# Performance work log

Measured on AMD Instinct MI355X. Metric: run time of the kernel, lower is better.

Reference implementation:

```python
import jax, jax.numpy as jnp
import numpy as np

L = 2000          # number of residues (sequence length)
FEATURES_L = 2048 # config.features_L pad target
W = 7             # config.window_size
D = 54            # per-residue feature dim after bert_lin
H = 3             # attention heads
HD = D // H       # head dim = 18
CH = 32           # conv hidden channels
KS = (3, 5, 7)    # config.kernels


def setup_inputs() -> dict:
    key = jax.random.key(0)
    ks = jax.random.split(key, 20)
    n = lambda k, s, sc=0.02: jax.random.normal(k, s, jnp.float32) * sc
    return {
        'beft_f': jax.random.normal(ks[0], (L, 1024), jnp.float32),
        'pssm_f': jax.random.normal(ks[1], (L, 20), jnp.float32),
        'hmm_f': jax.random.normal(ks[2], (L, 30), jnp.float32),
        'dssp_f': jax.random.normal(ks[3], (L, 14), jnp.float32),
        'W_bert': n(ks[4], (1024, D)), 'b_bert': jnp.zeros((D,), jnp.float32),
        'ln_g1': jnp.ones((D,), jnp.float32), 'ln_b1': jnp.zeros((D,), jnp.float32),
        'ln_g2': jnp.ones((D,), jnp.float32), 'ln_b2': jnp.zeros((D,), jnp.float32),
        'conv1_w': n(ks[5], (CH, 1, 3, 1), 0.1), 'conv1_b': n(ks[6], (CH,), 0.1),
        'prelu_a': jnp.array(0.25, jnp.float32),
        'conv2_w': n(ks[7], (CH, 1, 5, 1), 0.1), 'conv2_b': n(ks[8], (CH,), 0.1),
        'conv3_w': n(ks[9], (CH, 1, 7, 1), 0.1), 'conv3_b': n(ks[10], (CH,), 0.1),
        'W1': n(ks[11], (972, 256)), 'b1': jnp.zeros((256,), jnp.float32),
        'W2': n(ks[12], (CH * 256, 256)), 'b2': jnp.zeros((256,), jnp.float32),
    }


def _ln(x, g, b, eps=1e-5):
    m = x.mean(-1, keepdims=True)
    v = ((x - m) ** 2).mean(-1, keepdims=True)
    return (x - m) * jax.lax.rsqrt(v + eps) * g + b


def _attn(x, g, b):
    # x: (L, W, D); no qkv projections, no 1/sqrt(d) scaling (as in source)
    qh = x.reshape(x.shape[0], W, H, HD)
    s = jnp.einsum('bqhd,bkhd->bhqk', qh, qh)
    p = jax.nn.softmax(s, axis=-1)
    o = jnp.einsum('bhqk,bkhd->bqhd', p, qh).reshape(x.shape[0], W, D)
    return _ln(o, g, b)


def _conv_branch(x, w, bias, k, act):
    pad = (k - 1) // 2
    c = jax.lax.conv_general_dilated(x, w, (1, 1), ((pad, pad), (0, 0)),
                                     dimension_numbers=('NCHW', 'OIHW', 'NCHW'))
    c = act(c + bias[None, :, None, None])
    c = jax.lax.reduce_window(c, -jnp.inf, jax.lax.max,
                              (1, 1, k, 1), (1, 1, 1, 1), 'VALID')
    return c.reshape(c.shape[0], CH, -1)  # (FEATURES_L, 32, (W-k+1)*2D)


def _forward(beft_f, W_bert, b_bert, ln_g1, ln_b1, ln_g2, ln_b2,
             conv1_w, conv1_b, prelu_a, conv2_w, conv2_b, conv3_w, conv3_b,
             W1, b1, W2, b2):
    f = beft_f @ W_bert + b_bert  # (L, 54)
    # sliding-window gather replicating the source python loop exactly:
    # interior rows i in (W, L-W): window = f[i-4 : i+3]; boundary rows: [f[i], 0...0]
    i = jnp.arange(L)
    j = jnp.arange(W)
    gidx = jnp.clip(i[:, None] - (W // 2 + 1) + j[None, :], 0, L - 1)
    win_int = f[gidx]                                   # (L, 7, 54)
    win_bnd = jnp.zeros((L, W, D), f.dtype).at[:, 0].set(f)
    boundary = (i <= W) | (i + W >= L)
    new_f = jnp.where(boundary[:, None, None], win_bnd, win_int)
    sf = _attn(new_f, ln_g1, ln_b1)
    sf = _attn(sf, ln_g2, ln_b2)
    cat = jnp.concatenate([new_f, sf], axis=2)          # (L, 7, 108)
    x = jnp.pad(cat, ((0, FEATURES_L - L), (0, 0), (0, 0)))[:, None]  # (FL,1,7,108)
    prelu = lambda z: jnp.where(z >= 0, z, prelu_a * z)
    feats = jnp.concatenate([
        _conv_branch(x, conv1_w, conv1_b, KS[0], prelu),
        _conv_branch(x, conv2_w, conv2_b, KS[1], jax.nn.relu),
        _conv_branch(x, conv3_w, conv3_b, KS[2], jax.nn.relu)], axis=2)  # (FL,32,972)
    y = feats[:L] @ W1 + b1                             # (L, 32, 256)
    y = y.reshape(L, CH * 256) @ W2 + b2                # (L, 256)
    return jnp.where(y >= 0, y, 0.01 * y)               # leaky_relu


def reference(beft_f, pssm_f, hmm_f, dssp_f, W_bert, b_bert, ln_g1, ln_b1,
              ln_g2, ln_b2, conv1_w, conv1_b, prelu_a, conv2_w, conv2_b,
              conv3_w, conv3_b, W1, b1, W2, b2):
    # pssm_f / hmm_f / dssp_f are accepted but unused in the source forward
    return _forward(beft_f, W_bert, b_bert, ln_g1, ln_b1, ln_g2, ln_b2,
                    conv1_w, conv1_b, prelu_a, conv2_w, conv2_b,
                    conv3_w, conv3_b, W1, b1, W2, b2)
```

## Files before the change

### kernel.cpp

```cpp
#include <hip/hip_runtime.h>

#define L_RES 2000
#define DF 54
#define WIN 7

typedef short bf16x8 __attribute__((ext_vector_type(8)));
typedef float f32x4 __attribute__((ext_vector_type(4)));
typedef unsigned short ushort8v __attribute__((ext_vector_type(8)));

__device__ __forceinline__ unsigned short f2bf(float f) {
    unsigned int u = __float_as_uint(f);
    unsigned int r = (u + 0x7FFFu + ((u >> 16) & 1u)) >> 16;
    return (unsigned short)r;
}
__device__ __forceinline__ float bf2f(unsigned short h) {
    return __uint_as_float(((unsigned int)h) << 16);
}
__device__ __forceinline__ void gload16(const unsigned short* g, unsigned short* l) {
    __builtin_amdgcn_global_load_lds(
        (const __attribute__((address_space(1))) void*)g,
        (__attribute__((address_space(3))) void*)l, 16, 0, 0);
}

__global__ __launch_bounds__(256) void split_beft(const float* __restrict__ beft,
                                                  unsigned short* __restrict__ A2) {
    int l = blockIdx.x;
    int t = threadIdx.x;
    unsigned short* row = A2 + (size_t)l * 3072;
    for (int k = t; k < 1024; k += 256) {
        unsigned short hi = 0, lo = 0;
        if (l < L_RES) {
            float x = beft[(size_t)l * 1024 + k];
            hi = f2bf(x);
            lo = f2bf(x - bf2f(hi));
        }
        row[k] = hi;
        row[1024 + k] = lo;
        row[2048 + k] = hi;
    }
}

__global__ __launch_bounds__(256) void b2t_build(const float* __restrict__ Wb,
                                                 unsigned short* __restrict__ B2T) {
    int idx = blockIdx.x * 256 + threadIdx.x;
    int n = idx / 3072, col = idx % 3072;
    int seg = col >> 10, k = col & 1023;
    unsigned short r = 0;
    if (n < DF) {
        float v = Wb[(size_t)k * DF + n];
        unsigned short hi = f2bf(v);
        r = (seg < 2) ? hi : f2bf(v - bf2f(hi));
    }
    B2T[idx] = r;
}

__global__ __launch_bounds__(256) void bert_mfma(const unsigned short* __restrict__ A2,
                                                 const unsigned short* __restrict__ B2T,
                                                 float* __restrict__ bpart) {
    __shared__ unsigned short ldsA[128 * 64];
    __shared__ unsigned short ldsB[64 * 64];
    int t = threadIdx.x, w = t >> 6, lane = t & 63;
    int m0 = blockIdx.x * 128;
    int z = blockIdx.y;
    long koff = (long)z * 768;
    int wr = w >> 1, wc = w & 1;
    int arow = lane & 15, kgrp = lane >> 4;

    const unsigned short* aS[4]; const unsigned short* bS[2];
    int aD[4], bD[2];
    #pragma unroll
    for (int j = 0; j < 4; ++j) {
        int s = j * 256 + t, r = s >> 3, c = s & 7;
        aS[j] = A2 + koff + (size_t)(m0 + r) * 3072 + c * 8;
        aD[j] = r * 64 + ((c ^ (r & 7)) * 8);
    }
    #pragma unroll
    for (int j = 0; j < 2; ++j) {
        int s = j * 256 + t, r = s >> 3, c = s & 7;
        bS[j] = B2T + koff + (size_t)r * 3072 + c * 8;
        bD[j] = r * 64 + ((c ^ (r & 7)) * 8);
    }
    f32x4 acc[4][2];
    #pragma unroll
    for (int mi = 0; mi < 4; ++mi)
        #pragma unroll
        for (int ni = 0; ni < 2; ++ni) acc[mi][ni] = (f32x4)(0.f);

    ushort8v va[4], vb[2];
    #pragma unroll
    for (int j = 0; j < 4; ++j) va[j] = *(const ushort8v*)(aS[j]);
    #pragma unroll
    for (int j = 0; j < 2; ++j) vb[j] = *(const ushort8v*)(bS[j]);

    for (int ks = 0; ks < 12; ++ks) {
        __syncthreads();
        #pragma unroll
        for (int j = 0; j < 4; ++j) *(ushort8v*)&ldsA[aD[j]] = va[j];
        #pragma unroll
        for (int j = 0; j < 2; ++j) *(ushort8v*)&ldsB[bD[j]] = vb[j];
        __syncthreads();
        if (ks + 1 < 12) {
            #pragma unroll
            for (int j = 0; j < 4; ++j) va[j] = *(const ushort8v*)(aS[j] + (ks + 1) * 64);
            #pragma unroll
            for (int j = 0; j < 2; ++j) vb[j] = *(const ushort8v*)(bS[j] + (ks + 1) * 64);
        }
        #pragma unroll
        for (int kk = 0; kk < 2; ++kk) {
            int chunk = kk * 4 + kgrp;
            bf16x8 af[4], bfr[2];
            #pragma unroll
            for (int mi = 0; mi < 4; ++mi) {
                int rl = wr * 64 + mi * 16 + arow;
                af[mi] = *(const bf16x8*)&ldsA[rl * 64 + ((chunk ^ (rl & 7)) * 8)];
            }
            #pragma unroll
            for (int ni = 0; ni < 2; ++ni) {
                int rl = wc * 32 + ni * 16 + arow;
                bfr[ni] = *(const bf16x8*)&ldsB[rl * 64 + ((chunk ^ (rl & 7)) * 8)];
            }
            #pragma unroll
            for (int mi = 0; mi < 4; ++mi)
                #pragma unroll
                for (int ni = 0; ni < 2; ++ni)
                    acc[mi][ni] = __builtin_amdgcn_mfma_f32_16x16x32_bf16(af[mi], bfr[ni], acc[mi][ni], 0, 0, 0);
        }
    }
    #pragma unroll
    for (int ni = 0; ni < 2; ++ni) {
        int n = wc * 32 + ni * 16 + arow;
        #pragma unroll
        for (int mi = 0; mi < 4; ++mi)
            #pragma unroll
            for (int r = 0; r < 4; ++r) {
                int m = m0 + wr * 64 + mi * 16 + kgrp * 4 + r;
                bpart[((size_t)z * 2048 + m) * 64 + n] = acc[mi][ni][r];
            }
    }
}

__global__ __launch_bounds__(64) void bert_reduce(const float* __restrict__ bpart,
                                                  const float* __restrict__ bb,
                                                  float* __restrict__ f) {
    int l = blockIdx.x, n = threadIdx.x;
    if (n < DF) {
        float s = bb[n];
        #pragma unroll
        for (int z = 0; z < 4; ++z) s += bpart[((size_t)z * 2048 + l) * 64 + n];
        f[(size_t)l * DF + n] = s;
    }
}

__device__ __forceinline__ void attn_layer_w(const float (*in)[DF], float (*out)[DF],
                                             float (*s)[WIN][WIN],
                                             const float* __restrict__ g,
                                             const float* __restrict__ b,
                                             float* mm, float* vv, int lane) {
    for (int idx = lane; idx < 3 * WIN * WIN; idx += 64) {
        int h = idx / 49, r = idx % 49, q = r / WIN, k = r % WIN;
        float sum = 0.f;
        #pragma unroll
        for (int d = 0; d < 18; ++d) sum = fmaf(in[q][h * 18 + d], in[k][h * 18 + d], sum);
        s[h][q][k] = sum;
    }
    __syncthreads();
    for (int idx = lane; idx < 3 * WIN; idx += 64) {
        int h = idx / WIN, q = idx % WIN;
        float mx = s[h][q][0];
        #pragma unroll
        for (int k = 1; k < WIN; ++k) mx = fmaxf(mx, s[h][q][k]);
        float e[WIN], sum = 0.f;
        #pragma unroll
        for (int k = 0; k < WIN; ++k) { e[k] = expf(s[h][q][k] - mx); sum += e[k]; }
        float inv = 1.f / sum;
        #pragma unroll
        for (int k = 0; k < WIN; ++k) s[h][q][k] = e[k] * inv;
    }
    __syncthreads();
    for (int idx = lane; idx < WIN * DF; idx += 64) {
        int q = idx / DF, c = idx % DF, h = c / 18;
        float sum = 0.f;
        #pragma unroll
        for (int k = 0; k < WIN; ++k) sum = fmaf(s[h][q][k], in[k][c], sum);
        out[q][c] = sum;
    }
    __syncthreads();
    for (int q = lane; q < WIN; q += 64) {
        float m = 0.f;
        for (int c = 0; c < DF; ++c) m += out[q][c];
        m *= (1.f / DF);
        float v = 0.f;
        for (int c = 0; c < DF; ++c) { float d0 = out[q][c] - m; v = fmaf(d0, d0, v); }
        v *= (1.f / DF);
        mm[q] = m; vv[q] = rsqrtf(v + 1e-5f);
    }
    __syncthreads();
    for (int idx = lane; idx < WIN * DF; idx += 64) {
        int q = idx / DF, c = idx % DF;
        out[q][c] = (out[q][c] - mm[q]) * vv[q] * g[c] + b[c];
    }
    __syncthreads();
}

__global__ __launch_bounds__(256) void window_attn4(const float* __restrict__ f,
                                                    const float* __restrict__ g1,
                                                    const float* __restrict__ b1,
                                                    const float* __restrict__ g2,
                                                    const float* __restrict__ b2,
                                                    float* __restrict__ cat) {
    int wv = threadIdx.x >> 6, lane = threadIdx.x & 63;
    int l = blockIdx.x * 4 + wv;
    __shared__ float w[4][WIN][DF], o1[4][WIN][DF], o2[4][WIN][DF];
    __shared__ float s[4][3][WIN][WIN];
    __shared__ float mm[4][WIN], vvv[4][WIN];
    bool boundary = (l <= WIN) || (l + WIN >= L_RES);
    for (int idx = lane; idx < WIN * DF; idx += 64) {
        int j = idx / DF, d = idx % DF;
        w[wv][j][d] = boundary ? (j == 0 ? f[(size_t)l * DF + d] : 0.f)
                               : f[(size_t)(l - 4 + j) * DF + d];
    }
    __syncthreads();
    attn_layer_w(w[wv], o1[wv], s[wv], g1, b1, mm[wv], vvv[wv], lane);
    attn_layer_w(o1[wv], o2[wv], s[wv], g2, b2, mm[wv], vvv[wv], lane);
    for (int idx = lane; idx < WIN * DF; idx += 64) {
        int j = idx / DF, d = idx % DF;
        cat[(size_t)l * 756 + j * 108 + d] = w[wv][j][d];
        cat[(size_t)l * 756 + j * 108 + DF + d] = o2[wv][j][d];
    }
}

__global__ __launch_bounds__(256) void transpose_to_bf16(const float* __restrict__ src,
                                                         unsigned short* __restrict__ dst,
                                                         int M, int N, int Mpad) {
    __shared__ float tile[32][33];
    int m0 = blockIdx.x * 32, n0 = blockIdx.y * 32;
    int c = threadIdx.x % 32, r0 = threadIdx.x / 32;
    #pragma unroll
    for (int rr = 0; rr < 4; ++rr) {
        int r = r0 + rr * 8, m = m0 + r;
        tile[r][c] = (m < M) ? src[(size_t)m * N + n0 + c] : 0.f;
    }
    __syncthreads();
    #pragma unroll
    for (int rr = 0; rr < 4; ++rr) {
        int r = r0 + rr * 8;
        dst[(size_t)(n0 + r) * Mpad + m0 + c] = f2bf(tile[c][r]);
    }
}

__global__ __launch_bounds__(256) void zero_pad_rows(unsigned int* __restrict__ p) {
    int i = blockIdx.x * 256 + threadIdx.x;
    if (i < 196608) p[i] = 0u;
}

__global__ __launch_bounds__(256) void conv_pool(
        const float* __restrict__ cat,
        const float* __restrict__ c1w, const float* __restrict__ c1b,
        const float* __restrict__ pa_p,
        const float* __restrict__ c2w, const float* __restrict__ c2b,
        const float* __restrict__ c3w, const float* __restrict__ c3b,
        unsigned short* __restrict__ Ap, int lbase) {
    int l = lbase + blockIdx.x;
    int t = threadIdx.x;
    __shared__ float catl[756];
    __shared__ unsigned short Al[32 * 1024];
    for (int i = t; i < 756; i += 256) catl[i] = cat[(size_t)l * 756 + i];
    for (int i = t; i < 832; i += 256) {
        int r = i / 26, q = i - r * 26;
        *(unsigned int*)&Al[r * 1024 + 972 + q * 2] = 0u;
    }
    __syncthreads();
    float pa = pa_p[0];
    for (int idx = t; idx < 3456; idx += 256) {
        int c = idx / 108, d = idx - c * 108;
        unsigned short* Arow = Al + c * 1024;
        float col[WIN];
        #pragma unroll
        for (int h = 0; h < WIN; ++h) col[h] = catl[h * 108 + d];
        {
            float w0 = c1w[c * 3], w1 = c1w[c * 3 + 1], w2 = c1w[c * 3 + 2], bb = c1b[c];
            float v[WIN];
            #pragma unroll
            for (int h = 0; h < WIN; ++h) {
                float sum = bb;
                if (h >= 1) sum = fmaf(w0, col[h - 1], sum);
                sum = fmaf(w1, col[h], sum);
                if (h <= 5) sum = fmaf(w2, col[h + 1], sum);
                v[h] = sum >= 0.f ? sum : pa * sum;
            }
            #pragma unroll
            for (int p = 0; p < 5; ++p)
                Arow[p * 108 + d] = f2bf(fmaxf(fmaxf(v[p], v[p + 1]), v[p + 2]));
        }
        {
            float wg[5], bb = c2b[c];
            #pragma unroll
            for (int x = 0; x < 5; ++x) wg[x] = c2w[c * 5 + x];
            float v[WIN];
            #pragma unroll
            for (int h = 0; h < WIN; ++h) {
                float sum = bb;
                #pragma unroll
                for (int x = 0; x < 5; ++x) {
                    int hh = h + x - 2;
                    if (hh >= 0 && hh <= 6) sum = fmaf(wg[x], col[hh], sum);
                }
                v[h] = fmaxf(sum, 0.f);
            }
            #pragma unroll
            for (int p = 0; p < 3; ++p) {
                float mx = v[p];
                #pragma unroll
                for (int r = 1; r < 5; ++r) mx = fmaxf(mx, v[p + r]);
                Arow[540 + p * 108 + d] = f2bf(mx);
            }
        }
        {
            float wg[7], bb = c3b[c];
            #pragma unroll
            for (int x = 0; x < 7; ++x) wg[x] = c3w[c * 7 + x];
            float mx = 0.f;
            #pragma unroll
            for (int h = 0; h < WIN; ++h) {
                float sum = bb;
                #pragma unroll
                for (int x = 0; x < 7; ++x) {
                    int hh = h + x - 3;
                    if (hh >= 0 && hh <= 6) sum = fmaf(wg[x], col[hh], sum);
                }
                mx = fmaxf(mx, fmaxf(sum, 0.f));
            }
            Arow[864 + d] = f2bf(mx);
        }
    }
    __syncthreads();
    unsigned short* dst = Ap + (size_t)blockIdx.x * 32768;
    #pragma unroll
    for (int i = 0; i < 16; ++i) {
        int e = (i * 256 + t) * 8;
        *(ushort8v*)&dst[e] = *(const ushort8v*)&Al[e];
    }
}

template<bool EPI_BF16, int ZBITS>
__global__ __launch_bounds__(512) void gemm_tile8(
        const unsigned short* __restrict__ A, long lda,
        const unsigned short* __restrict__ B, long ldb,
        int nk, const float* __restrict__ bias,
        unsigned short* __restrict__ outB, float* __restrict__ outF,
        long outRowBase) {
    __shared__ unsigned short ldsA[128 * 64];
    __shared__ unsigned short ldsB[256 * 64];
    int t = threadIdx.x, w = t >> 6, lane = t & 63;
    int bid = blockIdx.x;
    int z = bid & ((1 << ZBITS) - 1);
    long m0 = (long)(bid >> ZBITS) * 128;
    long koff = (long)z * (long)nk * 64;
    A += koff; B += koff;
    int wr = w >> 2, wc = w & 3;
    int arow = lane & 15, kgrp = lane >> 4;
    int ra = lane >> 3, cc = lane & 7;
    int csw = (cc ^ ra) * 8;

    const unsigned short* gA[2]; const unsigned short* gB[4];
    unsigned short* dA[2]; unsigned short* dB[4];
    #pragma unroll
    for (int j = 0; j < 2; ++j) {
        int rbase = j * 64 + w * 8;
        gA[j] = A + (size_t)(m0 + rbase + ra) * lda + csw;
        dA[j] = &ldsA[rbase * 64];
    }
    #pragma unroll
    for (int j = 0; j < 4; ++j) {
        int rbase = j * 64 + w * 8;
        gB[j] = B + (size_t)(rbase + ra) * ldb + csw;
        dB[j] = &ldsB[rbase * 64];
    }
    f32x4 acc[4][4];
    #pragma unroll
    for (int mi = 0; mi < 4; ++mi)
        #pragma unroll
        for (int ni = 0; ni < 4; ++ni) acc[mi][ni] = (f32x4)(0.f);

    for (int ks = 0; ks < nk; ++ks) {
        #pragma unroll
        for (int j = 0; j < 2; ++j) gload16(gA[j] + ks * 64, dA[j]);
        #pragma unroll
        for (int j = 0; j < 4; ++j) gload16(gB[j] + ks * 64, dB[j]);
        __syncthreads();
        #pragma unroll
        for (int kk = 0; kk < 2; ++kk) {
            int chunk = kk * 4 + kgrp;
            bf16x8 af[4], bfr[4];
            #pragma unroll
            for (int mi = 0; mi < 4; ++mi) {
                int rl = wr * 64 + mi * 16 + arow;
                af[mi] = *(const bf16x8*)&ldsA[rl * 64 + ((chunk ^ (rl & 7)) * 8)];
            }
            #pragma unroll
            for (int ni = 0; ni < 4; ++ni) {
                int rl = wc * 64 + ni * 16 + arow;
                bfr[ni] = *(const bf16x8*)&ldsB[rl * 64 + ((chunk ^ (rl & 7)) * 8)];
            }
            #pragma unroll
            for (int mi = 0; mi < 4; ++mi)
                #pragma unroll
                for (int ni = 0; ni < 4; ++ni)
                    acc[mi][ni] = __builtin_amdgcn_mfma_f32_16x16x32_bf16(af[mi], bfr[ni], acc[mi][ni], 0, 0, 0);
        }
        __syncthreads();
    }
    #pragma unroll
    for (int ni = 0; ni < 4; ++ni) {
        int n = wc * 64 + ni * 16 + arow;
        float bv = EPI_BF16 ? bias[n] : 0.f;
        #pragma unroll
        for (int mi = 0; mi < 4; ++mi)
            #pragma unroll
            for (int r = 0; r < 4; ++r) {
                long m = m0 + wr * 64 + mi * 16 + kgrp * 4 + r;
                if (EPI_BF16)
                    outB[(outRowBase + m) * 256 + n] = f2bf(acc[mi][ni][r] + bv);
                else
                    outF[((long)z * 2048 + m) * 256 + n] = acc[mi][ni][r];
            }
    }
}

__global__ __launch_bounds__(256) void reduce2(const float* __restrict__ part,
                                               const float* __restrict__ b2v,
                                               float* __restrict__ out) {
    int l = blockIdx.x, n = threadIdx.x;
    float sum = b2v[n];
    #pragma unroll
    for (int s = 0; s < 8; ++s) sum += part[((size_t)s * 2048 + l) * 256 + n];
    out[(size_t)l * 256 + n] = sum >= 0.f ? sum : 0.01f * sum;
}

extern "C" void kernel_launch(void* const* d_in, const int* in_sizes, int n_in,
                              void* d_out, int out_size, void* d_ws, size_t ws_size,
                              hipStream_t stream) {
    const float* beft = (const float*)d_in[0];
    const float* Wb  = (const float*)d_in[4];
    const float* bb  = (const float*)d_in[5];
    const float* g1  = (const float*)d_in[6];
    const float* b1  = (const float*)d_in[7];
    const float* g2  = (const float*)d_in[8];
    const float* b2  = (const float*)d_in[9];
    const float* c1w = (const float*)d_in[10];
    const float* c1b = (const float*)d_in[11];
    const float* pa  = (const float*)d_in[12];
    const float* c2w = (const float*)d_in[13];
    const float* c2b = (const float*)d_in[14];
    const float* c3w = (const float*)d_in[15];
    const float* c3b = (const float*)d_in[16];
    const float* W1  = (const float*)d_in[17];
    const float* b1v = (const float*)d_in[18];
    const float* W2  = (const float*)d_in[19];
    const float* b2v = (const float*)d_in[20];
    float* out = (float*)d_out;
    char* ws = (char*)d_ws;

    float*          f    = (float*)(ws + 0);
    float*          cat  = (float*)(ws + 524288);
    unsigned short* W1T  = (unsigned short*)(ws + 8388608);
    unsigned short* W2T  = (unsigned short*)(ws + 8912896);
    unsigned short* y1   = (unsigned short*)(ws + 13107200);
    unsigned short* A2   = (unsigned short*)(ws + 13107200);
    unsigned short* B2T  = (unsigned short*)(ws + 25690112);
    float*          bpart= (float*)(ws + 46661632);
    unsigned short* Ap   = (unsigned short*)(ws + 46661632);
    float*          part = (float*)(ws + 46661632);

    long avail = (long)ws_size - 46661632L;
    long tpc = avail / (128L * 1024L * 2L);
    if (tpc < 1) tpc = 1;
    if (tpc > 500) tpc = 500;

    split_beft<<<2048, 256, 0, stream>>>(beft, A2);
    b2t_build<<<768, 256, 0, stream>>>(Wb, B2T);
    bert_mfma<<<dim3(16, 4), 256, 0, stream>>>(A2, B2T, bpart);
    bert_reduce<<<L_RES, 64, 0, stream>>>(bpart, bb, f);
    window_attn4<<<500, 256, 0, stream>>>(f, g1, b1, g2, b2, cat);
    transpose_to_bf16<<<dim3(32, 8), 256, 0, stream>>>(W1, W1T, 972, 256, 1024);
    transpose_to_bf16<<<dim3(256, 8), 256, 0, stream>>>(W2, W2T, 8192, 256, 8192);
    zero_pad_rows<<<768, 256, 0, stream>>>((unsigned int*)(y1 + (size_t)2000 * 8192));

    for (long t0 = 0; t0 < 500; t0 += tpc) {
        long nt = (500 - t0 < tpc) ? (500 - t0) : tpc;
        conv_pool<<<(int)(nt * 4), 256, 0, stream>>>(cat, c1w, c1b, pa, c2w, c2b,
                                                     c3w, c3b, Ap, (int)(t0 * 4));
        gemm_tile8<true, 0><<<(int)nt, 512, 0, stream>>>(
            Ap, 1024, W1T, 1024, 16, b1v, y1, nullptr, t0 * 128);
    }
    gemm_tile8<false, 3><<<128, 512, 0, stream>>>(
        y1, 8192, W2T, 8192, 16, nullptr, nullptr, part, 0);
    reduce2<<<L_RES, 256, 0, stream>>>(part, b2v, out);
}
```

Measured before the change: 169.4 us.

## Restructure conv_pool to process four residues per block with direct global writes

The conv/pool kernel now handles four residues per block. Each of 216 threads keeps two feature columns in registers and loops over all 32 channels, writing packed bf16 pairs straight to global memory instead of staging a 64KB LDS tile and copying it out. This drops the large shared-memory buffer and the extra copy pass, and reuses each loaded column across channels. In exchange it launches a quarter as many blocks (500 total), leaves 40 threads idle, and issues narrow 4-byte strided global stores.

```diff
diff --git a/kernel.cpp b/kernel.cpp
--- a/kernel.cpp
+++ b/kernel.cpp
@@ -260,85 +260,101 @@
         const float* __restrict__ c2w, const float* __restrict__ c2b,
         const float* __restrict__ c3w, const float* __restrict__ c3b,
         unsigned short* __restrict__ Ap, int lbase) {
-    int l = lbase + blockIdx.x;
+    int b = blockIdx.x;
+    int l0 = lbase + b * 4;
     int t = threadIdx.x;
-    __shared__ float catl[756];
-    __shared__ unsigned short Al[32 * 1024];
-    for (int i = t; i < 756; i += 256) catl[i] = cat[(size_t)l * 756 + i];
-    for (int i = t; i < 832; i += 256) {
+    __shared__ float catl[4 * 756];
+    for (int i = t; i < 3024; i += 256) catl[i] = cat[(size_t)l0 * 756 + i];
+    __syncthreads();
+    float pa = pa_p[0];
+    unsigned short* base = Ap + (size_t)b * 128 * 1024;
+    if (t < 216) {
+        int res = t / 54, dp = t - res * 54;
+        int d0 = dp * 2;
+        const float* cr = catl + res * 756;
+        float colA[WIN], colB[WIN];
+        #pragma unroll
+        for (int h = 0; h < WIN; ++h) {
+            colA[h] = cr[h * 108 + d0];
+            colB[h] = cr[h * 108 + d0 + 1];
+        }
+        for (int c = 0; c < 32; ++c) {
+            unsigned short* Arow = base + (size_t)(res * 32 + c) * 1024;
+            {
+                float w0 = c1w[c * 3], w1 = c1w[c * 3 + 1], w2 = c1w[c * 3 + 2];
+                float bb = c1b[c];
+                float vA[WIN], vB[WIN];
+                #pragma unroll
+                for (int h = 0; h < WIN; ++h) {
+                    float sA = bb, sB = bb;
+                    if (h >= 1) { sA = fmaf(w0, colA[h - 1], sA); sB = fmaf(w0, colB[h - 1], sB); }
+                    sA = fmaf(w1, colA[h], sA); sB = fmaf(w1, colB[h], sB);
+                    if (h <= 5) { sA = fmaf(w2, colA[h + 1], sA); sB = fmaf(w2, colB[h + 1], sB); }
+                    vA[h] = sA >= 0.f ? sA : pa * sA;
+                    vB[h] = sB >= 0.f ? sB : pa * sB;
+                }
+                #pragma unroll
+                for (int p = 0; p < 5; ++p) {
+                    unsigned int ua = f2bf(fmaxf(fmaxf(vA[p], vA[p + 1]), vA[p + 2]));
+                    unsigned int ub = f2bf(fmaxf(fmaxf(vB[p], vB[p + 1]), vB[p + 2]));
+                    *(unsigned int*)&Arow[p * 108 + d0] = ua | (ub << 16);
+                }
+            }
+            {
+                float wg[5], bb = c2b[c];
+                #pragma unroll
+                for (int x = 0; x < 5; ++x) wg[x] = c2w[c * 5 + x];
+                float vA[WIN], vB[WIN];
+                #pragma unroll
+                for (int h = 0; h < WIN; ++h) {
+                    float sA = bb, sB = bb;
+                    #pragma unroll
+                    for (int x = 0; x < 5; ++x) {
+                        int hh = h + x - 2;
+                        if (hh >= 0 && hh <= 6) {
+                            sA = fmaf(wg[x], colA[hh], sA);
+                            sB = fmaf(wg[x], colB[hh], sB);
+                        }
+                    }
+                    vA[h] = fmaxf(sA, 0.f);
+                    vB[h] = fmaxf(sB, 0.f);
+                }
+                #pragma unroll
+                for (int p = 0; p < 3; ++p) {
+                    float ma = vA[p], mb = vB[p];
+                    #pragma unroll
+                    for (int r = 1; r < 5; ++r) { ma = fmaxf(ma, vA[p + r]); mb = fmaxf(mb, vB[p + r]); }
+                    unsigned int ua = f2bf(ma), ub = f2bf(mb);
+                    *(unsigned int*)&Arow[540 + p * 108 + d0] = ua | (ub << 16);
+                }
+            }
+            {
+                float wg[7], bb = c3b[c];
+                #pragma unroll
+                for (int x = 0; x < 7; ++x) wg[x] = c3w[c * 7 + x];
+                float ma = 0.f, mb = 0.f;
+                #pragma unroll
+                for (int h = 0; h < WIN; ++h) {
+                    float sA = bb, sB = bb;
+                    #pragma unroll
+                    for (int x = 0; x < 7; ++x) {
+                        int hh = h + x - 3;
+                        if (hh >= 0 && hh <= 6) {
+                            sA = fmaf(wg[x], colA[hh], sA);
+                            sB = fmaf(wg[x], colB[hh], sB);
+                        }
+                    }
+                    ma = fmaxf(ma, sA);
+                    mb = fmaxf(mb, sB);
+                }
+                unsigned int ua = f2bf(fmaxf(ma, 0.f)), ub = f2bf(fmaxf(mb, 0.f));
+                *(unsigned int*)&Arow[864 + d0] = ua | (ub << 16);
+            }
+        }
+    }
+    for (int i = t; i < 3328; i += 256) {
         int r = i / 26, q = i - r * 26;
-        *(unsigned int*)&Al[r * 1024 + 972 + q * 2] = 0u;
-    }
-    __syncthreads();
-    float pa = pa_p[0];
-    for (int idx = t; idx < 3456; idx += 256) {
-        int c = idx / 108, d = idx - c * 108;
-        unsigned short* Arow = Al + c * 1024;
-        float col[WIN];
-        #pragma unroll
-        for (int h = 0; h < WIN; ++h) col[h] = catl[h * 108 + d];
-        {
-            float w0 = c1w[c * 3], w1 = c1w[c * 3 + 1], w2 = c1w[c * 3 + 2], bb = c1b[c];
-            float v[WIN];
-            #pragma unroll
-            for (int h = 0; h < WIN; ++h) {
-                float sum = bb;
-                if (h >= 1) sum = fmaf(w0, col[h - 1], sum);
-                sum = fmaf(w1, col[h], sum);
-                if (h <= 5) sum = fmaf(w2, col[h + 1], sum);
-                v[h] = sum >= 0.f ? sum : pa * sum;
-            }
-            #pragma unroll
-            for (int p = 0; p < 5; ++p)
-                Arow[p * 108 + d] = f2bf(fmaxf(fmaxf(v[p], v[p + 1]), v[p + 2]));
-        }
-        {
-            float wg[5], bb = c2b[c];
-            #pragma unroll
-            for (int x = 0; x < 5; ++x) wg[x] = c2w[c * 5 + x];
-            float v[WIN];
-            #pragma unroll
-            for (int h = 0; h < WIN; ++h) {
-                float sum = bb;
-                #pragma unroll
-                for (int x = 0; x < 5; ++x) {
-                    int hh = h + x - 2;
-                    if (hh >= 0 && hh <= 6) sum = fmaf(wg[x], col[hh], sum);
-                }
-                v[h] = fmaxf(sum, 0.f);
-            }
-            #pragma unroll
-            for (int p = 0; p < 3; ++p) {
-                float mx = v[p];
-                #pragma unroll
-                for (int r = 1; r < 5; ++r) mx = fmaxf(mx, v[p + r]);
-                Arow[540 + p * 108 + d] = f2bf(mx);
-            }
-        }
-        {
-            float wg[7], bb = c3b[c];
-            #pragma unroll
-            for (int x = 0; x < 7; ++x) wg[x] = c3w[c * 7 + x];
-            float mx = 0.f;
-            #pragma unroll
-            for (int h = 0; h < WIN; ++h) {
-                float sum = bb;
-                #pragma unroll
-                for (int x = 0; x < 7; ++x) {
-                    int hh = h + x - 3;
-                    if (hh >= 0 && hh <= 6) sum = fmaf(wg[x], col[hh], sum);
-                }
-                mx = fmaxf(mx, fmaxf(sum, 0.f));
-            }
-            Arow[864 + d] = f2bf(mx);
-        }
-    }
-    __syncthreads();
-    unsigned short* dst = Ap + (size_t)blockIdx.x * 32768;
-    #pragma unroll
-    for (int i = 0; i < 16; ++i) {
-        int e = (i * 256 + t) * 8;
-        *(ushort8v*)&dst[e] = *(const ushort8v*)&Al[e];
+        *(unsigned int*)&base[(size_t)r * 1024 + 972 + q * 2] = 0u;
     }
 }
 
@@ -488,8 +504,8 @@
 
     for (long t0 = 0; t0 < 500; t0 += tpc) {
         long nt = (500 - t0 < tpc) ? (500 - t0) : tpc;
-        conv_pool<<<(int)(nt * 4), 256, 0, stream>>>(cat, c1w, c1b, pa, c2w, c2b,
-                                                     c3w, c3b, Ap, (int)(t0 * 4));
+        conv_pool<<<(int)nt, 256, 0, stream>>>(cat, c1w, c1b, pa, c2w, c2b,
+                                               c3w, c3b, Ap, (int)(t0 * 4));
         gemm_tile8<true, 0><<<(int)nt, 512, 0, stream>>>(
             Ap, 1024, W1T, 1024, 16, b1v, y1, nullptr, t0 * 128);
     }
```

Result: faster. 159.4 us (-5.9%).
